# Kernel optimization log

Hardware: AMD Instinct MI355X
Metric: run time of the kernel (lower is better)

Reference implementation:

```python
import jax, jax.numpy as jnp
import numpy as np

N = 100000
E = 3200000
IN_CH, HID, OUT = 256, 64, 32


def setup_inputs() -> dict:
    key = jax.random.key(0)
    ks = jax.random.split(key, 8)
    x = jax.random.normal(ks[0], (N, IN_CH), dtype=jnp.float32)
    edge_index = jax.random.randint(ks[1], (2, E), 0, N, dtype=jnp.int64)
    # Glorot-ish init for weights, zeros for biases (PyG GCNConv: lin has no bias; conv bias added post-aggregation)
    W1 = jax.random.normal(ks[2], (IN_CH, HID), dtype=jnp.float32) / np.sqrt(IN_CH)
    b1 = jnp.zeros((HID,), dtype=jnp.float32)
    W2 = jax.random.normal(ks[3], (HID, OUT), dtype=jnp.float32) / np.sqrt(HID)
    b2 = jnp.zeros((OUT,), dtype=jnp.float32)
    Wc = jax.random.normal(ks[4], (OUT, 1), dtype=jnp.float32) / np.sqrt(OUT)
    bc = jnp.zeros((1,), dtype=jnp.float32)
    return {"x": x, "edge_index": edge_index, "W1": W1, "b1": b1,
            "W2": W2, "b2": b2, "Wc": Wc, "bc": bc}


def _gcn_norm(edge_index, num_nodes):
    # Add self-loops (PyG default), compute symmetric normalization D^{-1/2} A D^{-1/2}
    loops = jnp.arange(num_nodes, dtype=edge_index.dtype)
    row = jnp.concatenate([edge_index[0], loops])  # source
    col = jnp.concatenate([edge_index[1], loops])  # target (aggregation index)
    ones = jnp.ones(row.shape[0], dtype=jnp.float32)
    deg = jax.ops.segment_sum(ones, col, num_segments=num_nodes)
    dis = jnp.where(deg > 0, jax.lax.rsqrt(jnp.maximum(deg, 1e-12)), 0.0)
    norm = dis[row] * dis[col]  # [E+N]
    return row, col, norm


def _gcn_conv(x, W, b, row, col, norm, num_nodes):
    h = x @ W                                   # [N, F_out] dense transform first
    msg = h[row] * norm[:, None]                # gather + scale per edge
    agg = jax.ops.segment_sum(msg, col, num_segments=num_nodes)
    return agg + b


def reference(x, edge_index, W1, b1, W2, b2, Wc, bc):
    num_nodes = x.shape[0]
    row, col, norm = _gcn_norm(edge_index, num_nodes)
    h = jax.nn.elu(_gcn_conv(x, W1, b1, row, col, norm, num_nodes))
    h = jax.nn.elu(_gcn_conv(h, W2, b2, row, col, norm, num_nodes))
    return (h @ Wc + bc)[:, 0]                  # squeeze(1) -> [N]
```

## Files before the change

### kernel.cpp

```cpp
#include <hip/hip_runtime.h>
#include <hip/hip_fp16.h>
#include <math.h>

#define N_NODES 100000
#define N_EDGES 3200000
#define IN_CH   256
#define HID     64
#define OUTC    32
#define NBUCK   ((N_NODES + 127) / 128)
#define CHUNK   4096
#define EPT     16
#define CAP     4608

static constexpr size_t align256(size_t x) { return (x + 255) & ~(size_t)255; }
static constexpr size_t OFF_PTRB = 0;
static constexpr size_t OFF_PTRE = OFF_PTRB + align256((size_t)N_NODES * 4);
static constexpr size_t OFF_GCUR = OFF_PTRE + align256((size_t)N_NODES * 4);
static constexpr size_t OFF_DIS  = OFF_GCUR + align256((size_t)NBUCK * 4);
static constexpr size_t OFF_SRC  = OFF_DIS  + align256((size_t)N_NODES * 4);
static constexpr size_t OFF_PART = OFF_SRC  + align256((size_t)NBUCK * CAP * 4);
static constexpr size_t OFF_S1   = OFF_PART;
static constexpr size_t OFF_S2   = OFF_PART + align256((size_t)NBUCK * CAP * 4);

__device__ __forceinline__ void acc8(float* acc, float4 raw) {
    const __half2* hp = (const __half2*)&raw;
    float2 f0 = __half22float2(hp[0]);
    float2 f1 = __half22float2(hp[1]);
    float2 f2 = __half22float2(hp[2]);
    float2 f3 = __half22float2(hp[3]);
    acc[0] += f0.x; acc[1] += f0.y; acc[2] += f1.x; acc[3] += f1.y;
    acc[4] += f2.x; acc[5] += f2.y; acc[6] += f3.x; acc[7] += f3.y;
}

__global__ __launch_bounds__(256) void bucket_init(int* __restrict__ gcur) {
    int b = blockIdx.x * 256 + threadIdx.x;
    if (b < NBUCK) gcur[b] = b * CAP;
}

__global__ __launch_bounds__(256) void partition_edges(const int* __restrict__ row,
                                                       const int* __restrict__ col,
                                                       int* __restrict__ gcur,
                                                       int* __restrict__ part) {
    __shared__ int lhist[NBUCK];
    __shared__ int lbase[NBUCK];
    const int t  = threadIdx.x;
    const int e0 = blockIdx.x * CHUNK;
    for (int i = t; i < NBUCK; i += 256) lhist[i] = 0;
    __syncthreads();

    int pk[EPT], br[EPT];
#pragma unroll
    for (int i = 0; i < EPT; ++i) {
        int e = e0 + i * 256 + t;
        if (e < N_EDGES) {
            int d = col[e];
            int b = d >> 7;
            int r = atomicAdd(&lhist[b], 1);
            pk[i] = row[e] | ((d & 127) << 17);
            br[i] = b | (r << 10);
        } else {
            br[i] = -1;
        }
    }
    __syncthreads();

    const int off = (int)((blockIdx.x * 131u) % NBUCK);
    for (int i = t; i < NBUCK; i += 256) {
        int bb = i + off;
        if (bb >= NBUCK) bb -= NBUCK;
        int c = lhist[bb];
        lbase[bb] = (c > 0) ? atomicAdd(&gcur[bb], c) : 0;
    }
    __syncthreads();

#pragma unroll
    for (int i = 0; i < EPT; ++i) {
        if (br[i] >= 0) {
            int b = br[i] & 1023;
            int r = br[i] >> 10;
            part[lbase[b] + r] = pk[i];
        }
    }
}

__global__ __launch_bounds__(256) void bucket_build(const int* __restrict__ gcur,
                                                    const int* __restrict__ part,
                                                    int* __restrict__ ptrb,
                                                    int* __restrict__ ptre,
                                                    float* __restrict__ dis,
                                                    int* __restrict__ srcs) {
    __shared__ int lh[128];
    __shared__ int lb[128];
    __shared__ int lcur[128];
    const int b = blockIdx.x;
    const int t = threadIdx.x;
    if (t < 128) { lh[t] = 0; lcur[t] = 0; }
    __syncthreads();
    const int cnt = gcur[b] - b * CAP;
    const size_t pbase = (size_t)b * CAP;

    for (int i = t; i < cnt; i += 256)
        atomicAdd(&lh[part[pbase + i] >> 17], 1);
    __syncthreads();

    int val = (t < 128) ? lh[t] : 0;
    __shared__ int ls[128];
    if (t < 128) ls[t] = val;
    __syncthreads();
    for (int off = 1; off < 128; off <<= 1) {
        int add = (t >= off && t < 128) ? ls[t - off] : 0;
        __syncthreads();
        if (t < 128) ls[t] += add;
        __syncthreads();
    }
    if (t < 128) lb[t] = ls[t] - val;
    __syncthreads();

    int v = b * 128 + t;
    if (t < 128 && v < N_NODES) {
        ptrb[v] = b * CAP + lb[t];
        ptre[v] = b * CAP + lb[t] + val;
        dis[v]  = rsqrtf((float)val + 1.0f);
    }

    for (int i = t; i < cnt; i += 256) {
        int p    = part[pbase + i];
        int dlow = p >> 17;
        int src  = p & 0x1FFFF;
        int r    = atomicAdd(&lcur[dlow], 1);
        srcs[pbase + lb[dlow] + r] = src;
    }
}

__global__ __launch_bounds__(256) void gemm1(const float* __restrict__ x,
                                             const float* __restrict__ W1,
                                             const float* __restrict__ dis,
                                             __half* __restrict__ s1h) {
    __shared__ float wlds[64 * HID];
    __shared__ float xlds[64 * 68];

    const int t  = threadIdx.x;
    const int tx = t & 15;
    const int ty = t >> 4;
    const int row0 = blockIdx.x * 64;

    float acc[4][4] = {{0.f}};

    for (int kt = 0; kt < IN_CH / 64; ++kt) {
        {
            const float4* w4 = (const float4*)(W1 + (size_t)kt * 64 * HID);
            float4* l4 = (float4*)wlds;
#pragma unroll
            for (int i = 0; i < 4; ++i) l4[i * 256 + t] = w4[i * 256 + t];
        }
        {
#pragma unroll
            for (int i = 0; i < 4; ++i) {
                int L  = i * 256 + t;
                int rl = L >> 4;
                int k4 = L & 15;
                int rg = row0 + rl;
                float4 v;
                if (rg < N_NODES) v = ((const float4*)x)[(size_t)rg * 64 + kt * 16 + k4];
                else              v = make_float4(0.f, 0.f, 0.f, 0.f);
                *(float4*)(&xlds[rl * 68 + k4 * 4]) = v;
            }
        }
        __syncthreads();

        const float4* wl4 = (const float4*)wlds;
#pragma unroll 4
        for (int k4 = 0; k4 < 16; ++k4) {
            float4 xv[4];
#pragma unroll
            for (int i = 0; i < 4; ++i)
                xv[i] = *(const float4*)(&xlds[(ty * 4 + i) * 68 + k4 * 4]);
#pragma unroll
            for (int kk = 0; kk < 4; ++kk) {
                float4 bv = wl4[(k4 * 4 + kk) * 16 + tx];
#pragma unroll
                for (int i = 0; i < 4; ++i) {
                    const float* xf = (const float*)&xv[i];
                    float a = xf[kk];
                    acc[i][0] += a * bv.x;
                    acc[i][1] += a * bv.y;
                    acc[i][2] += a * bv.z;
                    acc[i][3] += a * bv.w;
                }
            }
        }
        __syncthreads();
    }

#pragma unroll
    for (int i = 0; i < 4; ++i) {
        int rr = row0 + ty * 4 + i;
        if (rr < N_NODES) {
            float d = dis[rr];
            __half2 p0 = __floats2half2_rn(acc[i][0] * d, acc[i][1] * d);
            __half2 p1 = __floats2half2_rn(acc[i][2] * d, acc[i][3] * d);
            __half2* dst = (__half2*)(s1h + (size_t)rr * HID + tx * 4);
            dst[0] = p0;
            dst[1] = p1;
        }
    }
}

__global__ __launch_bounds__(256) void gather1(const __half* __restrict__ s1h,
                                               const int* __restrict__ ptrb,
                                               const int* __restrict__ ptre,
                                               const int* __restrict__ srcs,
                                               const float* __restrict__ dis,
                                               const float* __restrict__ b1,
                                               const float* __restrict__ W2,
                                               __half* __restrict__ s2h) {
    __shared__ float w2lds[HID * OUTC];
    __shared__ float hbuf[4][HID];

    const int t = threadIdx.x;
    {
        float4* l4 = (float4*)w2lds;
        const float4* s4 = (const float4*)W2;
        l4[t] = s4[t];
        l4[256 + t] = s4[256 + t];
    }
    __syncthreads();

    const int j = t & 63;
    const int w = t >> 6;
    const int l = j & 31;
    const int h = j >> 5;
    const int v = __builtin_amdgcn_readfirstlane(blockIdx.x * 4 + w);
    const __half2* s12 = (const __half2*)s1h;

    float2 acc;
    {
        float2 self = __half22float2(s12[(v << 5) | l]);
        acc = (h == 0) ? self : make_float2(0.f, 0.f);
    }
    const int beg = ptrb[v];
    const int end = ptre[v];

    for (int base = beg; base < end; base += 64) {
        int mysrc = 0;
        if (base + j < end) mysrc = srcs[base + j];
        int nk = end - base;
        if (nk > 64) nk = 64;
        const int full = nk >> 1;
        int i = 0;
        for (; i + 8 <= full; i += 8) {
            int s  = 2 * i + h;
            int a0 = __shfl(mysrc, s,      64);
            int a1 = __shfl(mysrc, s + 2,  64);
            int a2 = __shfl(mysrc, s + 4,  64);
            int a3 = __shfl(mysrc, s + 6,  64);
            int a4 = __shfl(mysrc, s + 8,  64);
            int a5 = __shfl(mysrc, s + 10, 64);
            int a6 = __shfl(mysrc, s + 12, 64);
            int a7 = __shfl(mysrc, s + 14, 64);
            float2 g0 = __half22float2(s12[(a0 << 5) | l]);
            float2 g1 = __half22float2(s12[(a1 << 5) | l]);
            float2 g2 = __half22float2(s12[(a2 << 5) | l]);
            float2 g3 = __half22float2(s12[(a3 << 5) | l]);
            float2 g4 = __half22float2(s12[(a4 << 5) | l]);
            float2 g5 = __half22float2(s12[(a5 << 5) | l]);
            float2 g6 = __half22float2(s12[(a6 << 5) | l]);
            float2 g7 = __half22float2(s12[(a7 << 5) | l]);
            acc.x += ((g0.x + g1.x) + (g2.x + g3.x)) + ((g4.x + g5.x) + (g6.x + g7.x));
            acc.y += ((g0.y + g1.y) + (g2.y + g3.y)) + ((g4.y + g5.y) + (g6.y + g7.y));
        }
        if (2 * i < nk) {
            const int last = nk - 1;
#pragma unroll
            for (int u = 0; u < 8; ++u) {
                int s  = 2 * (i + u) + h;
                int sc = s < last ? s : last;
                int a  = __shfl(mysrc, sc, 64);
                float wgt = (s < nk) ? 1.f : 0.f;
                float2 g = __half22float2(s12[(a << 5) | l]);
                acc.x = fmaf(wgt, g.x, acc.x);
                acc.y = fmaf(wgt, g.y, acc.y);
            }
        }
    }
    acc.x += __shfl_xor(acc.x, 32, 64);
    acc.y += __shfl_xor(acc.y, 32, 64);

    float dv = dis[v];
    float2 bb = *(const float2*)(b1 + 2 * l);
    float t0 = dv * acc.x + bb.x;
    float t1 = dv * acc.y + bb.y;
    float h0 = t0 > 0.f ? t0 : (expf(t0) - 1.f);
    float h1 = t1 > 0.f ? t1 : (expf(t1) - 1.f);
    if (h == 0) {
        hbuf[w][2 * l]     = h0;
        hbuf[w][2 * l + 1] = h1;
    }

    const int jo = j & 31;
    const int kb = (j >> 5) * 32;
    float p = 0.f;
#pragma unroll
    for (int kk = 0; kk < 32; ++kk)
        p += hbuf[w][kb + kk] * w2lds[(kb + kk) * OUTC + jo];
    p += __shfl_xor(p, 32, 64);
    if (j < 32) {
        s2h[(size_t)v * OUTC + jo] = __float2half(dv * p);
    }
}

__global__ __launch_bounds__(256) void gather2(const __half* __restrict__ s2h,
                                               const int* __restrict__ ptrb,
                                               const int* __restrict__ ptre,
                                               const int* __restrict__ srcs,
                                               const float* __restrict__ dis,
                                               const float* __restrict__ b2,
                                               const float* __restrict__ Wc,
                                               const float* __restrict__ bc,
                                               float* __restrict__ out) {
    const int j = threadIdx.x & 63;
    const int w = threadIdx.x >> 6;
    const int l = j & 3;
    const int e = j >> 2;
    const int v = __builtin_amdgcn_readfirstlane(blockIdx.x * 4 + w);
    const float4* s24 = (const float4*)s2h;

    float acc[8] = {0.f, 0.f, 0.f, 0.f, 0.f, 0.f, 0.f, 0.f};
    if (e == 0) acc8(acc, s24[(v << 2) | l]);

    const int beg = ptrb[v];
    const int end = ptre[v];
    for (int base = beg; base < end; base += 64) {
        int mys = 0;
        if (base + j < end) mys = srcs[base + j];
        int nk = end - base;
        if (nk > 64) nk = 64;
        int off = 0;
        for (; off + 32 <= nk; off += 32) {
            int a0 = __shfl(mys, off + e,      64);
            int a1 = __shfl(mys, off + 16 + e, 64);
            float4 r0 = s24[(a0 << 2) | l];
            float4 r1 = s24[(a1 << 2) | l];
            acc8(acc, r0);
            acc8(acc, r1);
        }
        if (off < nk) {
            const int last = nk - 1;
            int s0 = off + e, s1 = off + 16 + e;
            int a0 = __shfl(mys, s0 < last ? s0 : last, 64);
            int a1 = __shfl(mys, s1 < last ? s1 : last, 64);
            if (s0 < nk) acc8(acc, s24[(a0 << 2) | l]);
            if (s1 < nk) acc8(acc, s24[(a1 << 2) | l]);
        }
    }
#pragma unroll
    for (int i = 0; i < 8; ++i) {
        acc[i] += __shfl_xor(acc[i], 4, 64);
        acc[i] += __shfl_xor(acc[i], 8, 64);
        acc[i] += __shfl_xor(acc[i], 16, 64);
        acc[i] += __shfl_xor(acc[i], 32, 64);
    }

    float dv = dis[v];
    float4 ba = ((const float4*)b2)[2 * l];
    float4 bb = ((const float4*)b2)[2 * l + 1];
    float4 wa = ((const float4*)Wc)[2 * l];
    float4 wb = ((const float4*)Wc)[2 * l + 1];
    const float* bf = (const float*)&ba;
    const float* bg = (const float*)&bb;
    const float* wf = (const float*)&wa;
    const float* wg = (const float*)&wb;
    float p = 0.f;
#pragma unroll
    for (int i = 0; i < 8; ++i) {
        float bias = (i < 4) ? bf[i] : bg[i - 4];
        float wc   = (i < 4) ? wf[i] : wg[i - 4];
        float tt = dv * acc[i] + bias;
        float hh = tt > 0.f ? tt : (expf(tt) - 1.f);
        p += hh * wc;
    }
    p += __shfl_xor(p, 1, 64);
    p += __shfl_xor(p, 2, 64);
    if (j == 0) out[v] = p + bc[0];
}

extern "C" void kernel_launch(void* const* d_in, const int* in_sizes, int n_in,
                              void* d_out, int out_size, void* d_ws, size_t ws_size,
                              hipStream_t stream) {
    const float* x  = (const float*)d_in[0];
    const int*   ei = (const int*)d_in[1];
    const float* W1 = (const float*)d_in[2];
    const float* b1 = (const float*)d_in[3];
    const float* W2 = (const float*)d_in[4];
    const float* b2 = (const float*)d_in[5];
    const float* Wc = (const float*)d_in[6];
    const float* bc = (const float*)d_in[7];
    float* out = (float*)d_out;

    const int* row = ei;
    const int* col = ei + N_EDGES;

    char* ws = (char*)d_ws;
    int*    ptrb = (int*)   (ws + OFF_PTRB);
    int*    ptre = (int*)   (ws + OFF_PTRE);
    int*    gcur = (int*)   (ws + OFF_GCUR);
    float*  dis  = (float*) (ws + OFF_DIS);
    int*    srcs = (int*)   (ws + OFF_SRC);
    int*    part = (int*)   (ws + OFF_PART);
    __half* s1h  = (__half*)(ws + OFF_S1);
    __half* s2h  = (__half*)(ws + OFF_S2);

    bucket_init    <<<(NBUCK + 255) / 256, 256, 0, stream>>>(gcur);
    partition_edges<<<(N_EDGES + CHUNK - 1) / CHUNK, 256, 0, stream>>>(row, col, gcur, part);
    bucket_build   <<<NBUCK, 256, 0, stream>>>(gcur, part, ptrb, ptre, dis, srcs);

    gemm1  <<<(N_NODES + 63) / 64, 256, 0, stream>>>(x, W1, dis, s1h);
    gather1<<<N_NODES / 4, 256, 0, stream>>>(s1h, ptrb, ptre, srcs, dis, b1, W2, s2h);
    gather2<<<N_NODES / 4, 256, 0, stream>>>(s2h, ptrb, ptre, srcs, dis, b2, Wc, bc, out);
}
```

Baseline: 394.4 us.

## Run first GCN dense transform on MFMA with split-fp16 precision emulation

Replaces the scalar FP32 tiled GEMM for x@W1 with a matrix-core path: inputs and weights are split into fp16 high and low parts and combined with three MFMA 16x16x32 calls per tile to approximate fp32 accuracy. Tiles become 128 rows per block with K chunks of 32. Output is staged through LDS for coalesced 16-byte stores. The intent is to cut the FMA-bound compute in gemm1, at the cost of conversion work, more LDS traffic and a small precision change.

Measured after the change: 374.3 us. 5.1% less time.

```diff
diff --git a/kernel.cpp b/kernel.cpp
--- a/kernel.cpp
+++ b/kernel.cpp
@@ -21,6 +21,10 @@
 static constexpr size_t OFF_PART = OFF_SRC  + align256((size_t)NBUCK * CAP * 4);
 static constexpr size_t OFF_S1   = OFF_PART;
 static constexpr size_t OFF_S2   = OFF_PART + align256((size_t)NBUCK * CAP * 4);
+
+typedef _Float16 f16;
+typedef f16 f16x8 __attribute__((ext_vector_type(8)));
+typedef float f32x4 __attribute__((ext_vector_type(4)));
 
 __device__ __forceinline__ void acc8(float* acc, float4 raw) {
     const __half2* hp = (const __half2*)&raw;
@@ -136,72 +140,107 @@
                                              const float* __restrict__ W1,
                                              const float* __restrict__ dis,
                                              __half* __restrict__ s1h) {
-    __shared__ float wlds[64 * HID];
-    __shared__ float xlds[64 * 68];
-
-    const int t  = threadIdx.x;
-    const int tx = t & 15;
-    const int ty = t >> 4;
-    const int row0 = blockIdx.x * 64;
-
-    float acc[4][4] = {{0.f}};
-
-    for (int kt = 0; kt < IN_CH / 64; ++kt) {
-        {
-            const float4* w4 = (const float4*)(W1 + (size_t)kt * 64 * HID);
-            float4* l4 = (float4*)wlds;
-#pragma unroll
-            for (int i = 0; i < 4; ++i) l4[i * 256 + t] = w4[i * 256 + t];
-        }
-        {
-#pragma unroll
-            for (int i = 0; i < 4; ++i) {
-                int L  = i * 256 + t;
-                int rl = L >> 4;
-                int k4 = L & 15;
-                int rg = row0 + rl;
-                float4 v;
-                if (rg < N_NODES) v = ((const float4*)x)[(size_t)rg * 64 + kt * 16 + k4];
-                else              v = make_float4(0.f, 0.f, 0.f, 0.f);
-                *(float4*)(&xlds[rl * 68 + k4 * 4]) = v;
+    __shared__ __align__(16) char lds_raw[30720];
+    f16* xh  = (f16*)lds_raw;
+    f16* xl  = (f16*)(lds_raw + 10240);
+    f16* wth = (f16*)(lds_raw + 20480);
+    f16* wtl = (f16*)(lds_raw + 25600);
+
+    const int t    = threadIdx.x;
+    const int row0 = blockIdx.x * 128;
+    const int lane = t & 63;
+    const int wv   = t >> 6;
+    const int lr   = lane & 15;
+    const int kg   = lane >> 4;
+
+    f32x4 acc[2][4];
+#pragma unroll
+    for (int m = 0; m < 2; ++m)
+#pragma unroll
+        for (int n = 0; n < 4; ++n) acc[m][n] = (f32x4){0.f, 0.f, 0.f, 0.f};
+
+    for (int kt = 0; kt < 8; ++kt) {
+#pragma unroll
+        for (int i = 0; i < 4; ++i) {
+            int L  = i * 256 + t;
+            int r  = L >> 3;
+            int k4 = L & 7;
+            int rg = row0 + r;
+            float4 v = make_float4(0.f, 0.f, 0.f, 0.f);
+            if (rg < N_NODES)
+                v = ((const float4*)x)[(size_t)rg * 64 + kt * 8 + k4];
+            union { f16 h[4]; unsigned long long u; } ph, pl;
+            const float* vf = (const float*)&v;
+#pragma unroll
+            for (int c = 0; c < 4; ++c) {
+                f16 hi = (f16)vf[c];
+                ph.h[c] = hi;
+                pl.h[c] = (f16)(vf[c] - (float)hi);
             }
+            *(unsigned long long*)(&xh[r * 40 + k4 * 4]) = ph.u;
+            *(unsigned long long*)(&xl[r * 40 + k4 * 4]) = pl.u;
+        }
+#pragma unroll
+        for (int i = 0; i < 2; ++i) {
+            int L  = i * 256 + t;
+            int k  = L >> 4;
+            int j4 = L & 15;
+            float4 v = ((const float4*)W1)[(size_t)(kt * 32 + k) * 16 + j4];
+            const float* vf = (const float*)&v;
+#pragma unroll
+            for (int c = 0; c < 4; ++c) {
+                f16 hi = (f16)vf[c];
+                wth[(j4 * 4 + c) * 40 + k] = hi;
+                wtl[(j4 * 4 + c) * 40 + k] = (f16)(vf[c] - (float)hi);
+            }
         }
         __syncthreads();
 
-        const float4* wl4 = (const float4*)wlds;
-#pragma unroll 4
-        for (int k4 = 0; k4 < 16; ++k4) {
-            float4 xv[4];
-#pragma unroll
-            for (int i = 0; i < 4; ++i)
-                xv[i] = *(const float4*)(&xlds[(ty * 4 + i) * 68 + k4 * 4]);
-#pragma unroll
-            for (int kk = 0; kk < 4; ++kk) {
-                float4 bv = wl4[(k4 * 4 + kk) * 16 + tx];
-#pragma unroll
-                for (int i = 0; i < 4; ++i) {
-                    const float* xf = (const float*)&xv[i];
-                    float a = xf[kk];
-                    acc[i][0] += a * bv.x;
-                    acc[i][1] += a * bv.y;
-                    acc[i][2] += a * bv.z;
-                    acc[i][3] += a * bv.w;
-                }
+        f16x8 ah[2], al[2], bh[4], bl[4];
+#pragma unroll
+        for (int m = 0; m < 2; ++m) {
+            ah[m] = *(const f16x8*)(&xh[(wv * 32 + m * 16 + lr) * 40 + kg * 8]);
+            al[m] = *(const f16x8*)(&xl[(wv * 32 + m * 16 + lr) * 40 + kg * 8]);
+        }
+#pragma unroll
+        for (int n = 0; n < 4; ++n) {
+            bh[n] = *(const f16x8*)(&wth[(n * 16 + lr) * 40 + kg * 8]);
+            bl[n] = *(const f16x8*)(&wtl[(n * 16 + lr) * 40 + kg * 8]);
+        }
+#pragma unroll
+        for (int m = 0; m < 2; ++m)
+#pragma unroll
+            for (int n = 0; n < 4; ++n) {
+                acc[m][n] = __builtin_amdgcn_mfma_f32_16x16x32_f16(ah[m], bh[n], acc[m][n], 0, 0, 0);
+                acc[m][n] = __builtin_amdgcn_mfma_f32_16x16x32_f16(ah[m], bl[n], acc[m][n], 0, 0, 0);
+                acc[m][n] = __builtin_amdgcn_mfma_f32_16x16x32_f16(al[m], bh[n], acc[m][n], 0, 0, 0);
             }
-        }
         __syncthreads();
     }
 
+    f16* ob = (f16*)lds_raw;
+#pragma unroll
+    for (int m = 0; m < 2; ++m) {
+#pragma unroll
+        for (int r = 0; r < 4; ++r) {
+            int rl = wv * 32 + m * 16 + kg * 4 + r;
+            int rg = row0 + rl;
+            float d = dis[rg < N_NODES ? rg : (N_NODES - 1)];
+#pragma unroll
+            for (int n = 0; n < 4; ++n)
+                ob[rl * 72 + n * 16 + lr] = (f16)(acc[m][n][r] * d);
+        }
+    }
+    __syncthreads();
 #pragma unroll
     for (int i = 0; i < 4; ++i) {
-        int rr = row0 + ty * 4 + i;
-        if (rr < N_NODES) {
-            float d = dis[rr];
-            __half2 p0 = __floats2half2_rn(acc[i][0] * d, acc[i][1] * d);
-            __half2 p1 = __floats2half2_rn(acc[i][2] * d, acc[i][3] * d);
-            __half2* dst = (__half2*)(s1h + (size_t)rr * HID + tx * 4);
-            dst[0] = p0;
-            dst[1] = p1;
+        int L = i * 256 + t;
+        int r = L >> 3;
+        int sg = L & 7;
+        int rg = row0 + r;
+        if (rg < N_NODES) {
+            f16x8 v = *(const f16x8*)(&ob[r * 72 + sg * 8]);
+            *(f16x8*)(s1h + (size_t)rg * HID + sg * 8) = v;
         }
     }
 }
@@ -414,7 +453,7 @@
     partition_edges<<<(N_EDGES + CHUNK - 1) / CHUNK, 256, 0, stream>>>(row, col, gcur, part);
     bucket_build   <<<NBUCK, 256, 0, stream>>>(gcur, part, ptrb, ptre, dis, srcs);
 
-    gemm1  <<<(N_NODES + 63) / 64, 256, 0, stream>>>(x, W1, dis, s1h);
+    gemm1  <<<(N_NODES + 127) / 128, 256, 0, stream>>>(x, W1, dis, s1h);
     gather1<<<N_NODES / 4, 256, 0, stream>>>(s1h, ptrb, ptre, srcs, dis, b1, W2, s2h);
     gather2<<<N_NODES / 4, 256, 0, stream>>>(s2h, ptrb, ptre, srcs, dis, b2, Wc, bc, out);
 }
```
